# Performance work log

Measured on AMD Instinct MI355X. Metric: run time of the kernel, lower is better.

The kernel has to match this reference:

```python
import jax, jax.numpy as jnp
import numpy as np


def _gcn_conv(x, W, b, src, dst, dinv):
    # PyG GCNConv: linear transform, then symmetric-normalized aggregation, then bias
    n = x.shape[0]
    h = x @ W  # [N, out]
    norm = (dinv[src] * dinv[dst])[:, None]  # [E, 1]
    msg = h[src] * norm  # gather + scale, [E, out]
    out = jax.ops.segment_sum(msg, dst, num_segments=n)  # scatter-add
    return out + b


def setup_inputs() -> dict:
    key = jax.random.key(0)
    k1, k2, k3, k4 = jax.random.split(key, 4)
    N, E, F_IN, F_HID, F_OUT = 50000, 800000, 512, 256, 64
    x = jax.random.normal(k1, (N, F_IN), dtype=jnp.float32)
    edge_index = jax.random.randint(k2, (2, E), 0, N, dtype=jnp.int64)
    # Glorot-ish init for weights
    W1 = jax.random.normal(k3, (F_IN, F_HID), dtype=jnp.float32) * (1.0 / np.sqrt(F_IN))
    b1 = jnp.zeros((F_HID,), dtype=jnp.float32)
    W2 = jax.random.normal(k4, (F_HID, F_OUT), dtype=jnp.float32) * (1.0 / np.sqrt(F_HID))
    b2 = jnp.zeros((F_OUT,), dtype=jnp.float32)
    return {"x": x, "edge_index": edge_index, "W1": W1, "b1": b1, "W2": W2, "b2": b2}


def reference(x, edge_index, W1, b1, W2, b2):
    n = x.shape[0]
    # Add self loops (GCNConv default)
    loop = jnp.arange(n, dtype=edge_index.dtype)
    src = jnp.concatenate([edge_index[0], loop])
    dst = jnp.concatenate([edge_index[1], loop])
    # Symmetric normalization D^{-1/2} (A+I) D^{-1/2}
    deg = jax.ops.segment_sum(jnp.ones_like(dst, dtype=x.dtype), dst, num_segments=n)
    dinv = jnp.where(deg > 0, jax.lax.rsqrt(deg), 0.0)
    h = _gcn_conv(x, W1, b1, src, dst, dinv)
    h = jax.nn.relu(h)
    # Dropout(p=0.5) is identity in eval mode (deterministic reference)
    h = _gcn_conv(h, W2, b2, src, dst, dinv)
    return jax.nn.log_softmax(h, axis=1)
```

## Files before the change

kernel.cpp:

```cpp
#include <hip/hip_runtime.h>
#include <math.h>

#define F_IN  512
#define F_HID 256
#define F_OUT 64

typedef __attribute__((ext_vector_type(8))) short bf16x8;
typedef __attribute__((ext_vector_type(4))) short bf16x4;
typedef __attribute__((ext_vector_type(4))) float f32x4;

#define GLOBAL_AS __attribute__((address_space(1)))
#define LDS_AS    __attribute__((address_space(3)))

__device__ __forceinline__ void gload_lds16(const ushort* g, ushort* l) {
    __builtin_amdgcn_global_load_lds((const GLOBAL_AS uint32_t*)g,
                                     (LDS_AS uint32_t*)l, 16, 0, 0);
}

__device__ __forceinline__ ushort f2bf(float f) {
    union { float f; uint32_t u; } v; v.f = f;
    uint32_t r = (v.u + 0x7FFFu + ((v.u >> 16) & 1u)) >> 16;
    return (ushort)r;
}

__device__ __forceinline__ float bf2f(ushort u) {
    union { uint32_t u; float f; } v; v.u = ((uint32_t)u) << 16;
    return v.f;
}

__device__ __forceinline__ bf16x8 conv8(float4 a, float4 b) {
    bf16x8 c;
    c[0] = (short)f2bf(a.x); c[1] = (short)f2bf(a.y);
    c[2] = (short)f2bf(a.z); c[3] = (short)f2bf(a.w);
    c[4] = (short)f2bf(b.x); c[5] = (short)f2bf(b.y);
    c[6] = (short)f2bf(b.z); c[7] = (short)f2bf(b.w);
    return c;
}

__global__ void k_deg(const int* __restrict__ dst, int* __restrict__ deg, int E) {
    int e = blockIdx.x * 256 + threadIdx.x;
    if (e < E) atomicAdd(&deg[dst[e]], 1);
}

__global__ void k_scan1(const int* __restrict__ deg, int* __restrict__ offs,
                        int* __restrict__ bsums, float* __restrict__ dinv, int N) {
    __shared__ int s[256];
    int tid = threadIdx.x;
    int i = blockIdx.x * 256 + tid;
    int v = (i < N) ? deg[i] : 0;
    if (i < N) dinv[i] = rsqrtf((float)(v + 1));
    s[tid] = v; __syncthreads();
    for (int d = 1; d < 256; d <<= 1) {
        int t = (tid >= d) ? s[tid - d] : 0;
        __syncthreads();
        s[tid] += t;
        __syncthreads();
    }
    if (i < N) offs[i] = s[tid] - v;
    if (tid == 255) bsums[blockIdx.x] = s[255];
}

__global__ void k_scan2(int* __restrict__ bsums, int n) {
    __shared__ int s[256];
    int tid = threadIdx.x;
    int v = (tid < n) ? bsums[tid] : 0;
    s[tid] = v; __syncthreads();
    for (int d = 1; d < 256; d <<= 1) {
        int t = (tid >= d) ? s[tid - d] : 0;
        __syncthreads();
        s[tid] += t;
        __syncthreads();
    }
    if (tid < n) bsums[tid] = s[tid] - v;
}

__global__ void k_scan3(int* __restrict__ offs, const int* __restrict__ bsums,
                        int* __restrict__ cursor, int2* __restrict__ jw, int N, int E) {
    int i = blockIdx.x * 256 + threadIdx.x;
    if (i < N) {
        int o = offs[i] + bsums[i >> 8];
        offs[i] = o;
        cursor[i] = o;
    }
    if (i == 0) offs[N] = E;
    if (i < 16) jw[E + i] = make_int2(0, 0);
}

__global__ void k_fill(const int* __restrict__ src, const int* __restrict__ dst,
                       int* __restrict__ cursor, int2* __restrict__ jw,
                       const float* __restrict__ dinv, int E) {
    int e = blockIdx.x * 256 + threadIdx.x;
    if (e < E) {
        int s = src[e];
        int pos = atomicAdd(&cursor[dst[e]], 1);
        jw[pos] = make_int2(s, __float_as_int(dinv[s]));
    }
}

__global__ void k_tcast2(const float* __restrict__ W1, ushort* __restrict__ w1t,
                         const float* __restrict__ W2, ushort* __restrict__ w2t) {
    int idx = blockIdx.x * 256 + threadIdx.x;
    const int n1 = F_IN * F_HID;
    if (idx < n1) {
        int n = idx / F_IN, k = idx - n * F_IN;
        w1t[idx] = f2bf(W1[(size_t)k * F_HID + n]);
    } else {
        int t = idx - n1;
        if (t < F_HID * F_OUT) {
            int n = t / F_HID, k = t - n * F_HID;
            w2t[t] = f2bf(W2[(size_t)k * F_OUT + n]);
        }
    }
}

__global__ __launch_bounds__(256) void k_gemm1(
        const float* __restrict__ A, const ushort* __restrict__ Bt,
        ushort* __restrict__ C, int M) {
    constexpr int K = F_IN, Nc = F_HID, BM = 64, BN = 64, NT = K / 32;
    constexpr int ASTR = 36;
    __shared__ ushort As[2][BM * ASTR];
    __shared__ ushort Bs[2][BN * 32];
    const int tid  = threadIdx.x;
    const int wave = tid >> 6, lane = tid & 63;
    const int wr = wave & 1, wc = wave >> 1;
    const int brow = blockIdx.y * BM, bcol = blockIdx.x * BN;

    f32x4 acc[2][2];
    #pragma unroll
    for (int m = 0; m < 2; ++m)
        #pragma unroll
        for (int n = 0; n < 2; ++n) acc[m][n] = (f32x4){0.f, 0.f, 0.f, 0.f};

    const int arow = tid >> 2;
    const int akc  = (tid & 3) * 8;
    int agrow = brow + arow; if (agrow >= M) agrow = M - 1;
    const float4* ap = (const float4*)&A[(size_t)agrow * K + akc];
    const int csrc = (tid & 3) ^ ((tid >> 3) & 3);
    const ushort* bp = &Bt[(size_t)(bcol + (tid >> 2)) * K + csrc * 8];

    const int kqA = (lane >> 4) * 8;
    const int kqB = ((lane >> 4) ^ ((lane >> 1) & 3)) * 8;
    const int rA0 = wr * 32 + (lane & 15);
    const int rB0 = wc * 32 + (lane & 15);

    float4 rg[2][2];

    rg[0][0] = ap[0]; rg[0][1] = ap[1];
    gload_lds16(bp, &Bs[0][wave * 512]);
    *(bf16x8*)&As[0][arow * ASTR + akc] = conv8(rg[0][0], rg[0][1]);
    rg[1][0] = ap[8]; rg[1][1] = ap[9];
    __syncthreads();

    #pragma unroll
    for (int t = 0; t < NT; ++t) {
        const int b = t & 1;
        if (t + 1 < NT) {
            gload_lds16(bp + (t + 1) * 32, &Bs[b ^ 1][wave * 512]);
            *(bf16x8*)&As[b ^ 1][arow * ASTR + akc] =
                conv8(rg[(t + 1) & 1][0], rg[(t + 1) & 1][1]);
        }
        if (t + 2 < NT) {
            rg[t & 1][0] = ap[(t + 2) * 8];
            rg[t & 1][1] = ap[(t + 2) * 8 + 1];
        }
        bf16x8 af[2], bfr[2];
        #pragma unroll
        for (int m = 0; m < 2; ++m)
            af[m] = *(const bf16x8*)&As[b][(rA0 + m * 16) * ASTR + kqA];
        #pragma unroll
        for (int n = 0; n < 2; ++n)
            bfr[n] = *(const bf16x8*)&Bs[b][(rB0 + n * 16) * 32 + kqB];
        #pragma unroll
        for (int m = 0; m < 2; ++m)
            #pragma unroll
            for (int n = 0; n < 2; ++n)
                acc[m][n] = __builtin_amdgcn_mfma_f32_16x16x32_bf16(af[m], bfr[n], acc[m][n], 0, 0, 0);
        if (t + 1 < NT) __syncthreads();
    }

    const int crow0 = brow + wr * 32 + (lane >> 4) * 4;
    const int ccol0 = bcol + wc * 32 + (lane & 15);
    #pragma unroll
    for (int m = 0; m < 2; ++m)
        #pragma unroll
        for (int n = 0; n < 2; ++n)
            #pragma unroll
            for (int j = 0; j < 4; ++j) {
                int row = crow0 + m * 16 + j;
                if (row < M) C[(size_t)row * Nc + ccol0 + n * 16] = f2bf(acc[m][n][j]);
            }
}

template<int WR, int WC, int MR, int NR>
__global__ __launch_bounds__(256) void k_gemm_bf16(
        const ushort* __restrict__ A, const ushort* __restrict__ Bt,
        ushort* __restrict__ C, int M, int K, int Nc) {
    constexpr int BM = WR * MR * 16;
    constexpr int BN = WC * NR * 16;
    __shared__ ushort As[BM * 32];
    __shared__ ushort Bs[BN * 32];
    const int tid  = threadIdx.x;
    const int wave = tid >> 6, lane = tid & 63;
    const int wr = wave % WR, wc = wave / WR;
    const int brow = blockIdx.y * BM, bcol = blockIdx.x * BN;

    f32x4 acc[MR][NR];
    #pragma unroll
    for (int m = 0; m < MR; ++m)
        #pragma unroll
        for (int n = 0; n < NR; ++n) acc[m][n] = (f32x4){0.f, 0.f, 0.f, 0.f};

    const int srow = tid >> 2;
    const int scol = (tid & 3) * 8;
    const int kq  = (lane >> 4) * 8;
    const int rA0 = wr * MR * 16 + (lane & 15);
    const int rB0 = wc * NR * 16 + (lane & 15);

    for (int k0 = 0; k0 < K; k0 += 32) {
        #pragma unroll
        for (int l = 0; l < BM / 64; ++l) {
            int row = brow + l * 64 + srow;
            if (row >= M) row = M - 1;
            gload_lds16(&A[(size_t)row * K + k0 + scol], &As[l * 2048 + wave * 512]);
        }
        #pragma unroll
        for (int l = 0; l < BN / 64; ++l) {
            int row = bcol + l * 64 + srow;
            gload_lds16(&Bt[(size_t)row * K + k0 + scol], &Bs[l * 2048 + wave * 512]);
        }
        __syncthreads();
        bf16x8 af[MR], bfr[NR];
        #pragma unroll
        for (int m = 0; m < MR; ++m)
            af[m] = *(const bf16x8*)&As[(rA0 + m * 16) * 32 + kq];
        #pragma unroll
        for (int n = 0; n < NR; ++n)
            bfr[n] = *(const bf16x8*)&Bs[(rB0 + n * 16) * 32 + kq];
        #pragma unroll
        for (int m = 0; m < MR; ++m)
            #pragma unroll
            for (int n = 0; n < NR; ++n)
                acc[m][n] = __builtin_amdgcn_mfma_f32_16x16x32_bf16(af[m], bfr[n], acc[m][n], 0, 0, 0);
        __syncthreads();
    }

    const int crow0 = brow + wr * MR * 16 + (lane >> 4) * 4;
    const int ccol0 = bcol + wc * NR * 16 + (lane & 15);
    #pragma unroll
    for (int m = 0; m < MR; ++m)
        #pragma unroll
        for (int n = 0; n < NR; ++n)
            #pragma unroll
            for (int j = 0; j < 4; ++j) {
                int row = crow0 + m * 16 + j;
                if (row < M) C[(size_t)row * Nc + ccol0 + n * 16] = f2bf(acc[m][n][j]);
            }
}

__global__ __launch_bounds__(256) void k_agg1(
        const ushort* __restrict__ h, const int2* __restrict__ jw,
        const int* __restrict__ offs, const float* __restrict__ dinv,
        const float* __restrict__ bias, ushort* __restrict__ outm, int N) {
    int wave = threadIdx.x >> 6, lane = threadIdx.x & 63;
    int i = blockIdx.x * 4 + wave;
    if (i >= N) return;
    int g = lane & 31;
    int p = lane >> 5;
    float di = dinv[i];
    float acc[8];
    {
        bf16x8 hv = *(const bf16x8*)&h[(size_t)i * F_HID + g * 8];
        float w = (p == 0) ? di * di : 0.f;
        #pragma unroll
        for (int k = 0; k < 8; ++k) acc[k] = bf2f((ushort)hv[k]) * w;
    }
    int s = offs[i], e = offs[i + 1];
    for (int u = s; u < e; u += 12) {
        int2 a[6];
        #pragma unroll
        for (int q = 0; q < 6; ++q) a[q] = jw[u + 2 * q + p];
        bf16x8 hv[6];
        #pragma unroll
        for (int q = 0; q < 6; ++q)
            hv[q] = *(const bf16x8*)&h[(size_t)a[q].x * F_HID + g * 8];
        #pragma unroll
        for (int q = 0; q < 6; ++q) {
            float ww = (u + 2 * q + p < e) ? __int_as_float(a[q].y) * di : 0.f;
            #pragma unroll
            for (int k = 0; k < 8; ++k) acc[k] += bf2f((ushort)hv[q][k]) * ww;
        }
    }
    #pragma unroll
    for (int k = 0; k < 8; ++k) acc[k] += __shfl_xor(acc[k], 32, 64);
    if (p == 0) {
        float4 b0 = *(const float4*)&bias[g * 8];
        float4 b1 = *(const float4*)&bias[g * 8 + 4];
        bf16x8 o;
        o[0] = (short)f2bf(fmaxf(acc[0] + b0.x, 0.f));
        o[1] = (short)f2bf(fmaxf(acc[1] + b0.y, 0.f));
        o[2] = (short)f2bf(fmaxf(acc[2] + b0.z, 0.f));
        o[3] = (short)f2bf(fmaxf(acc[3] + b0.w, 0.f));
        o[4] = (short)f2bf(fmaxf(acc[4] + b1.x, 0.f));
        o[5] = (short)f2bf(fmaxf(acc[5] + b1.y, 0.f));
        o[6] = (short)f2bf(fmaxf(acc[6] + b1.z, 0.f));
        o[7] = (short)f2bf(fmaxf(acc[7] + b1.w, 0.f));
        *(bf16x8*)&outm[(size_t)i * F_HID + g * 8] = o;
    }
}

__global__ __launch_bounds__(256) void k_agg2(
        const ushort* __restrict__ h, const int2* __restrict__ jw,
        const int* __restrict__ offs, const float* __restrict__ dinv,
        const float* __restrict__ bias, float* __restrict__ outm, int N) {
    int wave = threadIdx.x >> 6, lane = threadIdx.x & 63;
    int i = blockIdx.x * 4 + wave;
    if (i >= N) return;
    float di = dinv[i];
    float acc = bf2f(h[(size_t)i * F_OUT + lane]) * di * di;
    int s = offs[i], e = offs[i + 1];
    for (int u = s; u < e; u += 8) {
        int2 a[8];
        #pragma unroll
        for (int q = 0; q < 8; ++q) a[q] = jw[u + q];
        float hv[8];
        #pragma unroll
        for (int q = 0; q < 8; ++q)
            hv[q] = bf2f(h[(size_t)a[q].x * F_OUT + lane]);
        #pragma unroll
        for (int q = 0; q < 8; ++q) {
            float ww = (u + q < e) ? __int_as_float(a[q].y) * di : 0.f;
            acc += hv[q] * ww;
        }
    }
    acc += bias[lane];
    float m = acc;
    #pragma unroll
    for (int o = 32; o >= 1; o >>= 1) m = fmaxf(m, __shfl_xor(m, o, 64));
    float ex = expf(acc - m);
    float ssum = ex;
    #pragma unroll
    for (int o = 32; o >= 1; o >>= 1) ssum += __shfl_xor(ssum, o, 64);
    outm[(size_t)i * F_OUT + lane] = acc - m - logf(ssum);
}

extern "C" void kernel_launch(void* const* d_in, const int* in_sizes, int n_in,
                              void* d_out, int out_size, void* d_ws, size_t ws_size,
                              hipStream_t stream) {
    const float* x  = (const float*)d_in[0];
    const int*   ei = (const int*)d_in[1];
    const float* W1 = (const float*)d_in[2];
    const float* b1 = (const float*)d_in[3];
    const float* W2 = (const float*)d_in[4];
    const float* b2 = (const float*)d_in[5];
    float* out = (float*)d_out;

    int N = in_sizes[0] / F_IN;
    int E = in_sizes[1] / 2;
    const int* src = ei;
    const int* dst = ei + E;

    ushort* w1t = (ushort*)d_ws;
    ushort* w2t = w1t + F_HID * F_IN;
    ushort* h1  = w2t + F_OUT * F_HID;
    ushort* a1  = h1 + (size_t)N * F_HID;
    int*    deg = (int*)(a1 + (size_t)N * F_HID);
    float*  dinv = (float*)(deg + N);
    int*    offs = (int*)(dinv + N);
    int*    cursor = offs + N + 1;
    int*    bsums  = cursor + N;
    int2*   jw = (int2*)(((uintptr_t)(bsums + 256) + 7) & ~(uintptr_t)7);
    ushort* h2 = h1;

    int nch = (N + 255) / 256;

    hipMemsetAsync(deg, 0, sizeof(int) * N, stream);
    k_deg <<<(E + 255) / 256, 256, 0, stream>>>(dst, deg, E);
    k_scan1<<<nch, 256, 0, stream>>>(deg, offs, bsums, dinv, N);
    k_scan2<<<1, 256, 0, stream>>>(bsums, nch);
    k_scan3<<<nch, 256, 0, stream>>>(offs, bsums, cursor, jw, N, E);
    k_fill<<<(E + 255) / 256, 256, 0, stream>>>(src, dst, cursor, jw, dinv, E);

    int ntc = F_IN * F_HID + F_HID * F_OUT;
    k_tcast2<<<(ntc + 255) / 256, 256, 0, stream>>>(W1, w1t, W2, w2t);

    k_gemm1<<<dim3(F_HID / 64, (N + 63) / 64), 256, 0, stream>>>(x, w1t, h1, N);
    k_agg1<<<(N + 3) / 4, 256, 0, stream>>>(h1, jw, offs, dinv, b1, a1, N);

    k_gemm_bf16<4, 1, 1, 4><<<dim3(1, (N + 63) / 64), 256, 0, stream>>>(
        a1, w2t, h2, N, F_HID, F_OUT);
    k_agg2<<<(N + 3) / 4, 256, 0, stream>>>(h2, jw, offs, dinv, b2, out, N);
}
```

Measured before the change: 270.9 us.

## Drop LDS staging in both GEMMs, load MFMA fragments straight from global

Both GEMM kernels stop staging tiles through shared memory. Each lane now reads its MFMA A and B fragments directly from global memory, so the barriers and LDS traffic go away. GEMM1 widens its block to 128 output columns, giving each wave a 32x64 tile, and halves the grid in x. The cost is that x (fp32) is re-read and re-converted by two column blocks, weight fragments are loaded redundantly per wave, and the row-strided fragment reads coalesce poorly, so the kernels now depend on L1/L2 hits.

```diff
diff --git a/kernel.cpp b/kernel.cpp
--- a/kernel.cpp
+++ b/kernel.cpp
@@ -6,16 +6,7 @@
 #define F_OUT 64
 
 typedef __attribute__((ext_vector_type(8))) short bf16x8;
-typedef __attribute__((ext_vector_type(4))) short bf16x4;
 typedef __attribute__((ext_vector_type(4))) float f32x4;
-
-#define GLOBAL_AS __attribute__((address_space(1)))
-#define LDS_AS    __attribute__((address_space(3)))
-
-__device__ __forceinline__ void gload_lds16(const ushort* g, ushort* l) {
-    __builtin_amdgcn_global_load_lds((const GLOBAL_AS uint32_t*)g,
-                                     (LDS_AS uint32_t*)l, 16, 0, 0);
-}
 
 __device__ __forceinline__ ushort f2bf(float f) {
     union { float f; uint32_t u; } v; v.f = f;
@@ -116,74 +107,53 @@
 __global__ __launch_bounds__(256) void k_gemm1(
         const float* __restrict__ A, const ushort* __restrict__ Bt,
         ushort* __restrict__ C, int M) {
-    constexpr int K = F_IN, Nc = F_HID, BM = 64, BN = 64, NT = K / 32;
-    constexpr int ASTR = 36;
-    __shared__ ushort As[2][BM * ASTR];
-    __shared__ ushort Bs[2][BN * 32];
+    constexpr int K = F_IN, Nc = F_HID, BM = 64, NT = K / 32;
     const int tid  = threadIdx.x;
     const int wave = tid >> 6, lane = tid & 63;
     const int wr = wave & 1, wc = wave >> 1;
-    const int brow = blockIdx.y * BM, bcol = blockIdx.x * BN;
-
-    f32x4 acc[2][2];
+    const int brow = blockIdx.y * BM, bcol = blockIdx.x * 128;
+
+    const int l15 = lane & 15;
+    const int kq  = (lane >> 4) * 8;
+
+    int r0 = brow + wr * 32 + l15; if (r0 >= M) r0 = M - 1;
+    int r1 = r0 + 16;              if (r1 >= M) r1 = M - 1;
+    const float* a0p = &A[(size_t)r0 * K + kq];
+    const float* a1p = &A[(size_t)r1 * K + kq];
+    const ushort* bp0 = &Bt[(size_t)(bcol + wc * 64 + l15) * K + kq];
+
+    f32x4 acc[2][4];
     #pragma unroll
     for (int m = 0; m < 2; ++m)
         #pragma unroll
-        for (int n = 0; n < 2; ++n) acc[m][n] = (f32x4){0.f, 0.f, 0.f, 0.f};
-
-    const int arow = tid >> 2;
-    const int akc  = (tid & 3) * 8;
-    int agrow = brow + arow; if (agrow >= M) agrow = M - 1;
-    const float4* ap = (const float4*)&A[(size_t)agrow * K + akc];
-    const int csrc = (tid & 3) ^ ((tid >> 3) & 3);
-    const ushort* bp = &Bt[(size_t)(bcol + (tid >> 2)) * K + csrc * 8];
-
-    const int kqA = (lane >> 4) * 8;
-    const int kqB = ((lane >> 4) ^ ((lane >> 1) & 3)) * 8;
-    const int rA0 = wr * 32 + (lane & 15);
-    const int rB0 = wc * 32 + (lane & 15);
-
-    float4 rg[2][2];
-
-    rg[0][0] = ap[0]; rg[0][1] = ap[1];
-    gload_lds16(bp, &Bs[0][wave * 512]);
-    *(bf16x8*)&As[0][arow * ASTR + akc] = conv8(rg[0][0], rg[0][1]);
-    rg[1][0] = ap[8]; rg[1][1] = ap[9];
-    __syncthreads();
-
-    #pragma unroll
+        for (int n = 0; n < 4; ++n) acc[m][n] = (f32x4){0.f, 0.f, 0.f, 0.f};
+
+    #pragma unroll 4
     for (int t = 0; t < NT; ++t) {
-        const int b = t & 1;
-        if (t + 1 < NT) {
-            gload_lds16(bp + (t + 1) * 32, &Bs[b ^ 1][wave * 512]);
-            *(bf16x8*)&As[b ^ 1][arow * ASTR + akc] =
-                conv8(rg[(t + 1) & 1][0], rg[(t + 1) & 1][1]);
+        const int ko = t * 32;
+        float4 x00 = *(const float4*)(a0p + ko);
+        float4 x01 = *(const float4*)(a0p + ko + 4);
+        float4 x10 = *(const float4*)(a1p + ko);
+        float4 x11 = *(const float4*)(a1p + ko + 4);
+        bf16x8 bfr[4];
+        #pragma unroll
+        for (int n = 0; n < 4; ++n)
+            bfr[n] = *(const bf16x8*)(bp0 + (size_t)n * 16 * K + ko);
+        bf16x8 af0 = conv8(x00, x01);
+        bf16x8 af1 = conv8(x10, x11);
+        #pragma unroll
+        for (int n = 0; n < 4; ++n) {
+            acc[0][n] = __builtin_amdgcn_mfma_f32_16x16x32_bf16(af0, bfr[n], acc[0][n], 0, 0, 0);
+            acc[1][n] = __builtin_amdgcn_mfma_f32_16x16x32_bf16(af1, bfr[n], acc[1][n], 0, 0, 0);
         }
-        if (t + 2 < NT) {
-            rg[t & 1][0] = ap[(t + 2) * 8];
-            rg[t & 1][1] = ap[(t + 2) * 8 + 1];
-        }
-        bf16x8 af[2], bfr[2];
-        #pragma unroll
-        for (int m = 0; m < 2; ++m)
-            af[m] = *(const bf16x8*)&As[b][(rA0 + m * 16) * ASTR + kqA];
-        #pragma unroll
-        for (int n = 0; n < 2; ++n)
-            bfr[n] = *(const bf16x8*)&Bs[b][(rB0 + n * 16) * 32 + kqB];
-        #pragma unroll
-        for (int m = 0; m < 2; ++m)
-            #pragma unroll
-            for (int n = 0; n < 2; ++n)
-                acc[m][n] = __builtin_amdgcn_mfma_f32_16x16x32_bf16(af[m], bfr[n], acc[m][n], 0, 0, 0);
-        if (t + 1 < NT) __syncthreads();
     }
 
     const int crow0 = brow + wr * 32 + (lane >> 4) * 4;
-    const int ccol0 = bcol + wc * 32 + (lane & 15);
+    const int ccol0 = bcol + wc * 64 + l15;
     #pragma unroll
     for (int m = 0; m < 2; ++m)
         #pragma unroll
-        for (int n = 0; n < 2; ++n)
+        for (int n = 0; n < 4; ++n)
             #pragma unroll
             for (int j = 0; j < 4; ++j) {
                 int row = crow0 + m * 16 + j;
@@ -191,65 +161,49 @@
             }
 }
 
-template<int WR, int WC, int MR, int NR>
-__global__ __launch_bounds__(256) void k_gemm_bf16(
+__global__ __launch_bounds__(256) void k_gemm2(
         const ushort* __restrict__ A, const ushort* __restrict__ Bt,
-        ushort* __restrict__ C, int M, int K, int Nc) {
-    constexpr int BM = WR * MR * 16;
-    constexpr int BN = WC * NR * 16;
-    __shared__ ushort As[BM * 32];
-    __shared__ ushort Bs[BN * 32];
+        ushort* __restrict__ C, int M) {
+    constexpr int K = F_HID, Nc = F_OUT, BM = 64, NT = K / 32;
     const int tid  = threadIdx.x;
     const int wave = tid >> 6, lane = tid & 63;
-    const int wr = wave % WR, wc = wave / WR;
-    const int brow = blockIdx.y * BM, bcol = blockIdx.x * BN;
-
-    f32x4 acc[MR][NR];
-    #pragma unroll
-    for (int m = 0; m < MR; ++m)
-        #pragma unroll
-        for (int n = 0; n < NR; ++n) acc[m][n] = (f32x4){0.f, 0.f, 0.f, 0.f};
-
-    const int srow = tid >> 2;
-    const int scol = (tid & 3) * 8;
+    const int wr = wave & 1, wc = wave >> 1;
+    const int brow = blockIdx.y * BM;
+
+    const int l15 = lane & 15;
     const int kq  = (lane >> 4) * 8;
-    const int rA0 = wr * MR * 16 + (lane & 15);
-    const int rB0 = wc * NR * 16 + (lane & 15);
-
-    for (int k0 = 0; k0 < K; k0 += 32) {
-        #pragma unroll
-        for (int l = 0; l < BM / 64; ++l) {
-            int row = brow + l * 64 + srow;
-            if (row >= M) row = M - 1;
-            gload_lds16(&A[(size_t)row * K + k0 + scol], &As[l * 2048 + wave * 512]);
-        }
-        #pragma unroll
-        for (int l = 0; l < BN / 64; ++l) {
-            int row = bcol + l * 64 + srow;
-            gload_lds16(&Bt[(size_t)row * K + k0 + scol], &Bs[l * 2048 + wave * 512]);
-        }
-        __syncthreads();
-        bf16x8 af[MR], bfr[NR];
-        #pragma unroll
-        for (int m = 0; m < MR; ++m)
-            af[m] = *(const bf16x8*)&As[(rA0 + m * 16) * 32 + kq];
-        #pragma unroll
-        for (int n = 0; n < NR; ++n)
-            bfr[n] = *(const bf16x8*)&Bs[(rB0 + n * 16) * 32 + kq];
-        #pragma unroll
-        for (int m = 0; m < MR; ++m)
-            #pragma unroll
-            for (int n = 0; n < NR; ++n)
-                acc[m][n] = __builtin_amdgcn_mfma_f32_16x16x32_bf16(af[m], bfr[n], acc[m][n], 0, 0, 0);
-        __syncthreads();
-    }
-
-    const int crow0 = brow + wr * MR * 16 + (lane >> 4) * 4;
-    const int ccol0 = bcol + wc * NR * 16 + (lane & 15);
-    #pragma unroll
-    for (int m = 0; m < MR; ++m)
-        #pragma unroll
-        for (int n = 0; n < NR; ++n)
+
+    int r0 = brow + wr * 32 + l15; if (r0 >= M) r0 = M - 1;
+    int r1 = r0 + 16;              if (r1 >= M) r1 = M - 1;
+    const ushort* a0p = &A[(size_t)r0 * K + kq];
+    const ushort* a1p = &A[(size_t)r1 * K + kq];
+    const ushort* bp0 = &Bt[(size_t)(wc * 32 + l15) * K + kq];
+
+    f32x4 acc[2][2];
+    #pragma unroll
+    for (int m = 0; m < 2; ++m)
+        #pragma unroll
+        for (int n = 0; n < 2; ++n) acc[m][n] = (f32x4){0.f, 0.f, 0.f, 0.f};
+
+    #pragma unroll
+    for (int t = 0; t < NT; ++t) {
+        const int ko = t * 32;
+        bf16x8 af0 = *(const bf16x8*)(a0p + ko);
+        bf16x8 af1 = *(const bf16x8*)(a1p + ko);
+        bf16x8 b0  = *(const bf16x8*)(bp0 + ko);
+        bf16x8 b1  = *(const bf16x8*)(bp0 + (size_t)16 * K + ko);
+        acc[0][0] = __builtin_amdgcn_mfma_f32_16x16x32_bf16(af0, b0, acc[0][0], 0, 0, 0);
+        acc[0][1] = __builtin_amdgcn_mfma_f32_16x16x32_bf16(af0, b1, acc[0][1], 0, 0, 0);
+        acc[1][0] = __builtin_amdgcn_mfma_f32_16x16x32_bf16(af1, b0, acc[1][0], 0, 0, 0);
+        acc[1][1] = __builtin_amdgcn_mfma_f32_16x16x32_bf16(af1, b1, acc[1][1], 0, 0, 0);
+    }
+
+    const int crow0 = brow + wr * 32 + (lane >> 4) * 4;
+    const int ccol0 = wc * 32 + l15;
+    #pragma unroll
+    for (int m = 0; m < 2; ++m)
+        #pragma unroll
+        for (int n = 0; n < 2; ++n)
             #pragma unroll
             for (int j = 0; j < 4; ++j) {
                 int row = crow0 + m * 16 + j;
@@ -383,10 +337,9 @@
     int ntc = F_IN * F_HID + F_HID * F_OUT;
     k_tcast2<<<(ntc + 255) / 256, 256, 0, stream>>>(W1, w1t, W2, w2t);
 
-    k_gemm1<<<dim3(F_HID / 64, (N + 63) / 64), 256, 0, stream>>>(x, w1t, h1, N);
+    k_gemm1<<<dim3(2, (N + 63) / 64), 256, 0, stream>>>(x, w1t, h1, N);
     k_agg1<<<(N + 3) / 4, 256, 0, stream>>>(h1, jw, offs, dinv, b1, a1, N);
 
-    k_gemm_bf16<4, 1, 1, 4><<<dim3(1, (N + 63) / 64), 256, 0, stream>>>(
-        a1, w2t, h2, N, F_HID, F_OUT);
+    k_gemm2<<<dim3(1, (N + 63) / 64), 256, 0, stream>>>(a1, w2t, h2, N);
     k_agg2<<<(N + 3) / 4, 256, 0, stream>>>(h2, jw, offs, dinv, b2, out, N);
 }
```

New measurement: 323.8 us. +19.5%, slower.

## Triple-buffer GEMM1 with direct fp32 LDS loads and wider 64x128 tiles

Applied to the files above, without the earlier changes.

The first GEMM now loads fp32 activations straight into LDS with global_load_lds, using an XOR swizzle. The bf16 conversion moves to the LDS read path instead of going through registers. A three-stage buffer with explicit vmcnt waits and a single barrier per k-step replaces the double buffer. The tile widens to 128 columns so each wave issues more MFMAs per A fragment, and the grid drops to 2 column blocks. Separately, the layer-1 aggregation unrolls to 8 neighbors per lane pair to raise memory-level parallelism. The trade-off is more LDS per block (fp32 A, three stages), which may lower occupancy, plus extra conversion work on the compute side.

```diff
diff --git a/kernel.cpp b/kernel.cpp
--- a/kernel.cpp
+++ b/kernel.cpp
@@ -6,13 +6,12 @@
 #define F_OUT 64
 
 typedef __attribute__((ext_vector_type(8))) short bf16x8;
-typedef __attribute__((ext_vector_type(4))) short bf16x4;
 typedef __attribute__((ext_vector_type(4))) float f32x4;
 
 #define GLOBAL_AS __attribute__((address_space(1)))
 #define LDS_AS    __attribute__((address_space(3)))
 
-__device__ __forceinline__ void gload_lds16(const ushort* g, ushort* l) {
+__device__ __forceinline__ void gload_lds16(const void* g, void* l) {
     __builtin_amdgcn_global_load_lds((const GLOBAL_AS uint32_t*)g,
                                      (LDS_AS uint32_t*)l, 16, 0, 0);
 }
@@ -116,74 +115,83 @@
 __global__ __launch_bounds__(256) void k_gemm1(
         const float* __restrict__ A, const ushort* __restrict__ Bt,
         ushort* __restrict__ C, int M) {
-    constexpr int K = F_IN, Nc = F_HID, BM = 64, BN = 64, NT = K / 32;
-    constexpr int ASTR = 36;
-    __shared__ ushort As[2][BM * ASTR];
-    __shared__ ushort Bs[2][BN * 32];
+    constexpr int K = F_IN, Nc = F_HID, NT = K / 32;
+    __shared__ float  Asf[3][64 * 32];
+    __shared__ ushort Bsm[3][128 * 32];
     const int tid  = threadIdx.x;
     const int wave = tid >> 6, lane = tid & 63;
     const int wr = wave & 1, wc = wave >> 1;
-    const int brow = blockIdx.y * BM, bcol = blockIdx.x * BN;
-
-    f32x4 acc[2][2];
+    const int brow = blockIdx.y * 64, bcol = blockIdx.x * 128;
+    const int l15 = lane & 15, hi = lane >> 4;
+
+    const int aslot = tid & 7;
+    const int arow0 = tid >> 3;
+    const int kf = (((aslot * 16) ^ ((arow0 & 7) << 4)) >> 2);
+    int ar0 = brow + arow0;      if (ar0 >= M) ar0 = M - 1;
+    int ar1 = brow + arow0 + 32; if (ar1 >= M) ar1 = M - 1;
+    const float* ap0 = &A[(size_t)ar0 * K + kf];
+    const float* ap1 = &A[(size_t)ar1 * K + kf];
+    const int csrc = (tid & 3) ^ ((tid >> 3) & 3);
+    const ushort* bp0 = &Bt[(size_t)(bcol + (tid >> 2)) * K + csrc * 8];
+    const ushort* bp1 = &Bt[(size_t)(bcol + 64 + (tid >> 2)) * K + csrc * 8];
+
+    f32x4 acc[2][4];
     #pragma unroll
     for (int m = 0; m < 2; ++m)
         #pragma unroll
-        for (int n = 0; n < 2; ++n) acc[m][n] = (f32x4){0.f, 0.f, 0.f, 0.f};
-
-    const int arow = tid >> 2;
-    const int akc  = (tid & 3) * 8;
-    int agrow = brow + arow; if (agrow >= M) agrow = M - 1;
-    const float4* ap = (const float4*)&A[(size_t)agrow * K + akc];
-    const int csrc = (tid & 3) ^ ((tid >> 3) & 3);
-    const ushort* bp = &Bt[(size_t)(bcol + (tid >> 2)) * K + csrc * 8];
-
-    const int kqA = (lane >> 4) * 8;
-    const int kqB = ((lane >> 4) ^ ((lane >> 1) & 3)) * 8;
-    const int rA0 = wr * 32 + (lane & 15);
-    const int rB0 = wc * 32 + (lane & 15);
-
-    float4 rg[2][2];
-
-    rg[0][0] = ap[0]; rg[0][1] = ap[1];
-    gload_lds16(bp, &Bs[0][wave * 512]);
-    *(bf16x8*)&As[0][arow * ASTR + akc] = conv8(rg[0][0], rg[0][1]);
-    rg[1][0] = ap[8]; rg[1][1] = ap[9];
-    __syncthreads();
+        for (int n = 0; n < 4; ++n) acc[m][n] = (f32x4){0.f, 0.f, 0.f, 0.f};
+
+    #define STAGE1(buf, t)                                                        \
+        do {                                                                      \
+            const int _k0 = (t) * 32;                                             \
+            gload_lds16(ap0 + _k0, &Asf[buf][(0 * 256 + wave * 64) * 4]);         \
+            gload_lds16(ap1 + _k0, &Asf[buf][(1 * 256 + wave * 64) * 4]);         \
+            gload_lds16(bp0 + _k0, &Bsm[buf][(0 * 256 + wave * 64) * 8]);         \
+            gload_lds16(bp1 + _k0, &Bsm[buf][(1 * 256 + wave * 64) * 8]);         \
+        } while (0)
+
+    STAGE1(0, 0);
+    STAGE1(1, 1);
+
+    const int swA = (l15 & 7) << 4;
+    const int kbB = (hi ^ ((l15 >> 1) & 3)) * 16;
 
     #pragma unroll
     for (int t = 0; t < NT; ++t) {
-        const int b = t & 1;
-        if (t + 1 < NT) {
-            gload_lds16(bp + (t + 1) * 32, &Bs[b ^ 1][wave * 512]);
-            *(bf16x8*)&As[b ^ 1][arow * ASTR + akc] =
-                conv8(rg[(t + 1) & 1][0], rg[(t + 1) & 1][1]);
-        }
-        if (t + 2 < NT) {
-            rg[t & 1][0] = ap[(t + 2) * 8];
-            rg[t & 1][1] = ap[(t + 2) * 8 + 1];
-        }
-        bf16x8 af[2], bfr[2];
-        #pragma unroll
-        for (int m = 0; m < 2; ++m)
-            af[m] = *(const bf16x8*)&As[b][(rA0 + m * 16) * ASTR + kqA];
-        #pragma unroll
-        for (int n = 0; n < 2; ++n)
-            bfr[n] = *(const bf16x8*)&Bs[b][(rB0 + n * 16) * 32 + kqB];
+        if (t < NT - 1) asm volatile("s_waitcnt vmcnt(4)" ::: "memory");
+        else            asm volatile("s_waitcnt vmcnt(0)" ::: "memory");
+        __builtin_amdgcn_s_barrier();
+        __builtin_amdgcn_sched_barrier(0);
+        if (t + 2 < NT) STAGE1((t + 2) % 3, t + 2);
+        const int buf = t % 3;
+        bf16x8 af[2], bfr[4];
+        #pragma unroll
+        for (int m = 0; m < 2; ++m) {
+            const int row = wr * 32 + l15 + m * 16;
+            const char* base = (const char*)&Asf[buf][row * 32];
+            float4 f0 = *(const float4*)(base + ((hi * 32) ^ swA));
+            float4 f1 = *(const float4*)(base + ((hi * 32 + 16) ^ swA));
+            af[m] = conv8(f0, f1);
+        }
+        #pragma unroll
+        for (int n = 0; n < 4; ++n) {
+            const int row = wc * 64 + l15 + n * 16;
+            bfr[n] = *(const bf16x8*)((const char*)&Bsm[buf][row * 32] + kbB);
+        }
         #pragma unroll
         for (int m = 0; m < 2; ++m)
             #pragma unroll
-            for (int n = 0; n < 2; ++n)
+            for (int n = 0; n < 4; ++n)
                 acc[m][n] = __builtin_amdgcn_mfma_f32_16x16x32_bf16(af[m], bfr[n], acc[m][n], 0, 0, 0);
-        if (t + 1 < NT) __syncthreads();
-    }
-
-    const int crow0 = brow + wr * 32 + (lane >> 4) * 4;
-    const int ccol0 = bcol + wc * 32 + (lane & 15);
+    }
+    #undef STAGE1
+
+    const int crow0 = brow + wr * 32 + hi * 4;
+    const int ccol0 = bcol + wc * 64 + l15;
     #pragma unroll
     for (int m = 0; m < 2; ++m)
         #pragma unroll
-        for (int n = 0; n < 2; ++n)
+        for (int n = 0; n < 4; ++n)
             #pragma unroll
             for (int j = 0; j < 4; ++j) {
                 int row = crow0 + m * 16 + j;
@@ -275,16 +283,16 @@
         for (int k = 0; k < 8; ++k) acc[k] = bf2f((ushort)hv[k]) * w;
     }
     int s = offs[i], e = offs[i + 1];
-    for (int u = s; u < e; u += 12) {
-        int2 a[6];
-        #pragma unroll
-        for (int q = 0; q < 6; ++q) a[q] = jw[u + 2 * q + p];
-        bf16x8 hv[6];
-        #pragma unroll
-        for (int q = 0; q < 6; ++q)
+    for (int u = s; u < e; u += 16) {
+        int2 a[8];
+        #pragma unroll
+        for (int q = 0; q < 8; ++q) a[q] = jw[u + 2 * q + p];
+        bf16x8 hv[8];
+        #pragma unroll
+        for (int q = 0; q < 8; ++q)
             hv[q] = *(const bf16x8*)&h[(size_t)a[q].x * F_HID + g * 8];
         #pragma unroll
-        for (int q = 0; q < 6; ++q) {
+        for (int q = 0; q < 8; ++q) {
             float ww = (u + 2 * q + p < e) ? __int_as_float(a[q].y) * di : 0.f;
             #pragma unroll
             for (int k = 0; k < 8; ++k) acc[k] += bf2f((ushort)hv[q][k]) * ww;
@@ -383,7 +391,7 @@
     int ntc = F_IN * F_HID + F_HID * F_OUT;
     k_tcast2<<<(ntc + 255) / 256, 256, 0, stream>>>(W1, w1t, W2, w2t);
 
-    k_gemm1<<<dim3(F_HID / 64, (N + 63) / 64), 256, 0, stream>>>(x, w1t, h1, N);
+    k_gemm1<<<dim3(2, (N + 63) / 64), 256, 0, stream>>>(x, w1t, h1, N);
     k_agg1<<<(N + 3) / 4, 256, 0, stream>>>(h1, jw, offs, dinv, b1, a1, N);
 
     k_gemm_bf16<4, 1, 1, 4><<<dim3(1, (N + 63) / 64), 256, 0, stream>>>(
```

New measurement: 265.4 us. 2.0% less time.
